# Performance work log

Measured on AMD Instinct MI355X. Metric: run time of the kernel, lower is better.

Reference implementation:

```python
import jax, jax.numpy as jnp
import numpy as np

N_NODES = 100000
N_EDGES = 2000000


def _init_mlp(key, dims, scale=0.05):
    Ws, bs = [], []
    ks = jax.random.split(key, len(dims) - 1)
    for k, di, do in zip(ks, dims[:-1], dims[1:]):
        Ws.append(jax.random.normal(k, (di, do), dtype=jnp.float32) * scale)
        bs.append(jnp.zeros((do,), dtype=jnp.float32))
    return Ws, bs


def setup_inputs() -> dict:
    key = jax.random.key(0)
    ks = jax.random.split(key, 7)
    d = {
        "t": jax.random.uniform(ks[0], (1,), dtype=jnp.float32),
        "x": jax.random.normal(ks[1], (N_NODES, 4), dtype=jnp.float32),
        "Ofixed": jax.random.normal(ks[2], (N_NODES, 2), dtype=jnp.float32),
        "src_idx": jax.random.randint(ks[3], (N_EDGES,), 0, N_NODES, dtype=jnp.int32),
        "tgt_idx": jax.random.randint(ks[4], (N_EDGES,), 0, N_NODES, dtype=jnp.int32),
    }
    # fR: (2*d_O+1)=13 -> [150]*4 -> 50 ; fO: 50 -> [100] -> 4
    R_Ws, R_bs = _init_mlp(ks[5], [13, 150, 150, 150, 150, 50])
    O_Ws, O_bs = _init_mlp(ks[6], [50, 100, 4])
    for i, (W, b) in enumerate(zip(R_Ws, R_bs)):
        d[f"fR_W{i}"] = W
        d[f"fR_b{i}"] = b
    for i, (W, b) in enumerate(zip(O_Ws, O_bs)):
        d[f"fO_W{i}"] = W
        d[f"fO_b{i}"] = b
    return d


def _mlp(h, Ws, bs):
    # hidden layers with ReLU, linear output (matches MLP in the torch code)
    for W, b in zip(Ws[:-1], bs[:-1]):
        h = jax.nn.relu(h @ W + b)
    return h @ Ws[-1] + bs[-1]


def reference(t, x, Ofixed, src_idx, tgt_idx,
              fR_W0, fR_b0, fR_W1, fR_b1, fR_W2, fR_b2, fR_W3, fR_b3, fR_W4, fR_b4,
              fO_W0, fO_b0, fO_W1, fO_b1):
    O = jnp.concatenate([x, Ofixed], axis=1)            # [N, d_O]
    # Msrc.T @ O and Mtgt.T @ O with 0/1 incidence matrices == gathers
    Rsrc = O[src_idx]                                   # [M, d_O]
    Rtgt = O[tgt_idx]                                   # [M, d_O]
    tt = jnp.broadcast_to(t.reshape(1, 1).astype(O.dtype), (src_idx.shape[0], 1))
    R_prime = jnp.concatenate([Rsrc, Rtgt, tt], axis=1)  # [M, 2*d_O+1]
    E = _mlp(R_prime, [fR_W0, fR_W1, fR_W2, fR_W3, fR_W4],
             [fR_b0, fR_b1, fR_b2, fR_b3, fR_b4])        # [M, d_E]
    # Mtgt @ E == scatter-add of edge messages onto target nodes
    E_prime = jax.ops.segment_sum(E, tgt_idx, num_segments=x.shape[0])  # [N, d_E]
    P = _mlp(E_prime, [fO_W0, fO_W1], [fO_b0, fO_b1])    # [N, d_P]
    return P
```

## Files before the change

kernel.cpp:

```cpp
#include <hip/hip_runtime.h>
#include <hip/hip_bf16.h>

typedef unsigned short u16;
typedef __attribute__((ext_vector_type(8))) short short8;
typedef __attribute__((ext_vector_type(4))) float f32x4;

constexpr int SA     = 168;
constexpr int BLK_E  = 64;
constexpr int NTHR   = 192;
constexpr int CHUNK  = 512;
constexpr int WSLOT  = 50 * CHUNK;
constexpr size_t WT_BYTES = 5ull * WSLOT * 2;
constexpr size_t WS_HDR   = 262144;

constexpr int Ls (int s) { return s == 0 ? 0 : (s <= 15 ? 1 + (s - 1) / 5 : 4); }
constexpr int Kss(int s) { return s == 0 ? 0 : (s <= 15 ? (s - 1) % 5 : s - 16); }

__device__ __forceinline__ u16 f2bf(float f) {
    union { float f; unsigned u; } c; c.f = f;
    return (u16)((c.u + 0x7fffu + ((c.u >> 16) & 1u)) >> 16);
}
__device__ __forceinline__ unsigned pk_bf16(float a, float b) {
    float2 f; f.x = a; f.y = b;
    __hip_bfloat162 h = __float22bfloat162_rn(f);
    return *(unsigned*)&h;
}

__device__ __forceinline__ int kperm(int kp) {
    if (kp < 64)  return (kp & 3) * 16 + (kp >> 2);
    if (kp < 128) { const int m = kp - 64;  return (4 + (m & 3)) * 16 + (m >> 2); }
    if (kp < 160) { const int m = kp - 128; return (8 + (m & 1)) * 16 + (m >> 1); }
    return 1 << 30;
}

__global__ void prep_all(const float* __restrict__ W0, const float* __restrict__ W1,
                         const float* __restrict__ W2, const float* __restrict__ W3,
                         const float* __restrict__ W4,
                         const float* __restrict__ B0, const float* __restrict__ B1,
                         const float* __restrict__ B2, const float* __restrict__ B3,
                         const float* __restrict__ B4,
                         u16* __restrict__ Wt, float* __restrict__ Bp)
{
    const int l = blockIdx.y;
    if (l == 5) {
        const int idx = blockIdx.x * blockDim.x + threadIdx.x;
        if (idx < 800) {
            const int ll = idx / 160, j = idx - ll * 160;
            const float* B; int DO;
            if      (ll == 0) { B = B0; DO = 150; }
            else if (ll == 1) { B = B1; DO = 150; }
            else if (ll == 2) { B = B2; DO = 150; }
            else if (ll == 3) { B = B3; DO = 150; }
            else              { B = B4; DO = 50;  }
            Bp[idx] = (j < DO) ? B[j] : 0.f;
        }
        return;
    }
    const float* W; int DI, DO; bool perm;
    if      (l == 0) { W = W0; DI = 13;  DO = 150; perm = false; }
    else if (l == 1) { W = W1; DI = 150; DO = 150; perm = true;  }
    else if (l == 2) { W = W2; DI = 150; DO = 150; perm = true;  }
    else if (l == 3) { W = W3; DI = 150; DO = 150; perm = true;  }
    else             { W = W4; DI = 150; DO = 50;  perm = true;  }
    u16* dst = Wt + (size_t)l * WSLOT;
    for (int idx = blockIdx.x * blockDim.x + threadIdx.x; idx < WSLOT;
         idx += gridDim.x * blockDim.x) {
        const int chunk = idx / CHUNK;
        const int within = idx - chunk * CHUNK;
        const int lane = within >> 3, e = within & 7;
        const int ks = chunk / 10, j = chunk - ks * 10;
        const int c = lane & 15, q = lane >> 4;
        const int n = j * 16 + c;
        const int kphys = ks * 32 + q * 8 + e;
        const int klog = perm ? kperm(kphys) : kphys;
        const float v = (n < DO && klog < DI) ? W[klog * DO + n] : 0.f;
        dst[idx] = f2bf(v);
    }
}

__device__ __forceinline__ void loadB(const u16* __restrict__ Wt, int s,
                                      int wv, int lane, short8 (&slot)[4])
{
    const int l = Ls(s), ks = Kss(s);
    const int jb = (l < 4) ? wv * 4 : 0;
    const int nt = (l < 4 && wv == 2) ? 2 : 4;
    const u16* base = Wt + (size_t)l * WSLOT + (size_t)(ks * 10 + jb) * CHUNK + lane * 8;
#pragma unroll
    for (int jj = 0; jj < 4; ++jj)
        if (jj < nt) slot[jj] = *(const short8*)&base[jj * CHUNK];
}

__device__ __forceinline__ void epilogue(u16* act, const float* __restrict__ Bp,
                                         int l, int wv, int col, int quad,
                                         f32x4 (&acc)[4][4])
{
    const int jb = wv * 4;
    float bb[4];
#pragma unroll
    for (int jj = 0; jj < 4; ++jj) bb[jj] = Bp[l * 160 + (jb + jj) * 16 + col];
#pragma unroll
    for (int mt = 0; mt < 4; ++mt)
#pragma unroll
        for (int r = 0; r < 4; ++r) {
            u16* row = &act[(mt * 16 + quad * 4 + r) * SA];
            if (wv < 2) {
                uint2 pk;
                pk.x = pk_bf16(fmaxf(acc[mt][0][r] + bb[0], 0.f),
                               fmaxf(acc[mt][1][r] + bb[1], 0.f));
                pk.y = pk_bf16(fmaxf(acc[mt][2][r] + bb[2], 0.f),
                               fmaxf(acc[mt][3][r] + bb[3], 0.f));
                *(uint2*)&row[wv * 64 + col * 4] = pk;
            } else {
                *(unsigned*)&row[128 + col * 2] =
                    pk_bf16(fmaxf(acc[mt][0][r] + bb[0], 0.f),
                            fmaxf(acc[mt][1][r] + bb[1], 0.f));
            }
        }
}

__global__ __launch_bounds__(NTHR, 3) void edge_kernel(
    const float* __restrict__ t, const float* __restrict__ x, const float* __restrict__ Ofx,
    const int* __restrict__ src, const int* __restrict__ tgt,
    const u16* __restrict__ Wt, const float* __restrict__ Bp,
    float* __restrict__ Ep, int n_edges, int copy_mask, size_t copy_elems)
{
    __shared__ __align__(16) u16 act[BLK_E * SA];
    __shared__ int tgt_s[BLK_E];

    const int tid  = threadIdx.x;
    const int lane = tid & 63;
    const int wv   = tid >> 6;
    const int col  = lane & 15;
    const int quad = lane >> 4;

    const int xcd = (int)(__builtin_amdgcn_s_getreg(6164) & 7u) & copy_mask;
    float* __restrict__ Epc = Ep + (size_t)xcd * copy_elems;

    short8 Bwin[3][4];
    loadB(Wt, 0, wv, lane, Bwin[0]);
    loadB(Wt, 1, wv, lane, Bwin[1]);
    loadB(Wt, 2, wv, lane, Bwin[2]);

    if (tid < BLK_E) {
        const int e = tid;
        const long long ge = (long long)blockIdx.x * BLK_E + e;
        const bool valid = ge < n_edges;
        const int s = valid ? src[ge] : 0;
        const int g = valid ? tgt[ge] : 0;
        const float4 xs = valid ? *(const float4*)&x[(size_t)s * 4] : float4{0, 0, 0, 0};
        const float2 os = valid ? *(const float2*)&Ofx[(size_t)s * 2] : float2{0, 0};
        const float4 xg = valid ? *(const float4*)&x[(size_t)g * 4] : float4{0, 0, 0, 0};
        const float2 og = valid ? *(const float2*)&Ofx[(size_t)g * 2] : float2{0, 0};
        const float tv = valid ? t[0] : 0.f;
        uint4 w0, w1;
        w0.x = pk_bf16(xs.x, xs.y); w0.y = pk_bf16(xs.z, xs.w);
        w0.z = pk_bf16(os.x, os.y); w0.w = pk_bf16(xg.x, xg.y);
        w1.x = pk_bf16(xg.z, xg.w); w1.y = pk_bf16(og.x, og.y);
        w1.z = pk_bf16(tv, 0.f);    w1.w = 0u;
        u16* row = &act[e * SA];
        *(uint4*)&row[0]  = w0;
        *(uint4*)&row[8]  = w1;
        *(uint4*)&row[16] = uint4{0, 0, 0, 0};
        *(uint4*)&row[24] = uint4{0, 0, 0, 0};
        tgt_s[e] = valid ? g : -1;
    }
    __syncthreads();

    const int ntw = (wv == 2) ? 2 : 4;
    f32x4 acc[4][4];
    short8 Af[4];

#pragma unroll
    for (int mt = 0; mt < 4; ++mt)
#pragma unroll
        for (int jj = 0; jj < 4; ++jj) acc[mt][jj] = f32x4{0.f, 0.f, 0.f, 0.f};
#pragma unroll
    for (int mt = 0; mt < 4; ++mt)
        Af[mt] = *(const short8*)&act[(mt * 16 + col) * SA + quad * 8];
#pragma unroll
    for (int jj = 0; jj < 4; ++jj)
        if (jj < ntw)
#pragma unroll
            for (int mt = 0; mt < 4; ++mt)
                acc[mt][jj] = __builtin_amdgcn_mfma_f32_16x16x32_bf16(
                    Af[mt], Bwin[0][jj], acc[mt][jj], 0, 0, 0);
    loadB(Wt, 3, wv, lane, Bwin[0]);
    __syncthreads();
    epilogue(act, Bp, 0, wv, col, quad, acc);
    __syncthreads();

#pragma unroll
    for (int s = 1; s <= 15; ++s) {
        const int l = 1 + (s - 1) / 5;
        const int ks = (s - 1) % 5;
        const int slot = s % 3;
        if (ks == 0) {
#pragma unroll
            for (int mt = 0; mt < 4; ++mt)
#pragma unroll
                for (int jj = 0; jj < 4; ++jj) acc[mt][jj] = f32x4{0.f, 0.f, 0.f, 0.f};
        }
#pragma unroll
        for (int mt = 0; mt < 4; ++mt)
            Af[mt] = *(const short8*)&act[(mt * 16 + col) * SA + ks * 32 + quad * 8];
#pragma unroll
        for (int jj = 0; jj < 4; ++jj)
            if (jj < ntw)
#pragma unroll
                for (int mt = 0; mt < 4; ++mt)
                    acc[mt][jj] = __builtin_amdgcn_mfma_f32_16x16x32_bf16(
                        Af[mt], Bwin[slot][jj], acc[mt][jj], 0, 0, 0);
        if (s + 3 <= 20) loadB(Wt, s + 3, wv, lane, Bwin[slot]);
        if (ks == 4) {
            __syncthreads();
            epilogue(act, Bp, l, wv, col, quad, acc);
            __syncthreads();
        }
    }

    const int mb  = (wv == 0) ? 0 : wv + 1;
    const int nmt = (wv == 0) ? 2 : 1;
    f32x4 acc4[2][4];
#pragma unroll
    for (int k = 0; k < 2; ++k)
#pragma unroll
        for (int jj = 0; jj < 4; ++jj) acc4[k][jj] = f32x4{0.f, 0.f, 0.f, 0.f};
#pragma unroll
    for (int s = 16; s <= 20; ++s) {
        const int ks = s - 16;
        const int slot = s % 3;
        short8 A4[2];
#pragma unroll
        for (int k = 0; k < 2; ++k)
            if (k < nmt)
                A4[k] = *(const short8*)&act[((mb + k) * 16 + col) * SA + ks * 32 + quad * 8];
#pragma unroll
        for (int jj = 0; jj < 4; ++jj)
#pragma unroll
            for (int k = 0; k < 2; ++k)
                if (k < nmt)
                    acc4[k][jj] = __builtin_amdgcn_mfma_f32_16x16x32_bf16(
                        A4[k], Bwin[slot][jj], acc4[k][jj], 0, 0, 0);
        if (s + 3 <= 20) loadB(Wt, s + 3, wv, lane, Bwin[slot]);
    }

#pragma unroll
    for (int jj = 0; jj < 4; ++jj) {
        const int n = jj * 16 + col;
        if (n < 50) {
            const float bb = Bp[4 * 160 + n];
#pragma unroll
            for (int k = 0; k < 2; ++k)
                if (k < nmt)
#pragma unroll
                    for (int r = 0; r < 4; ++r) {
                        const int g = tgt_s[(mb + k) * 16 + quad * 4 + r];
                        if (g >= 0) atomicAdd(&Epc[(size_t)g * 50 + n], acc4[k][jj][r] + bb);
                    }
        }
    }
}

template<int DI, int DO, bool RELU>
__device__ __forceinline__ void mlp_layer_t(
    const float* __restrict__ W, const float* __restrict__ B,
    float (*in)[64], float (*out)[64], int tid)
{
    const int et = tid & 15;
    const int jt = tid >> 4;
    constexpr int NG = (DO + 15) / 16;

    float acc0[NG], acc1[NG], acc2[NG], acc3[NG];
#pragma unroll
    for (int g = 0; g < NG; ++g) {
        const int j = jt + 16 * g;
        const float bb = (j < DO) ? B[j] : 0.f;
        acc0[g] = bb; acc1[g] = bb; acc2[g] = bb; acc3[g] = bb;
    }
    for (int k = 0; k < DI; ++k) {
        const float4 a = *(const float4*)&in[k][et * 4];
#pragma unroll
        for (int g = 0; g < NG; ++g) {
            const int j = jt + 16 * g;
            const float wv = (j < DO) ? W[k * DO + j] : 0.f;
            acc0[g] = fmaf(a.x, wv, acc0[g]);
            acc1[g] = fmaf(a.y, wv, acc1[g]);
            acc2[g] = fmaf(a.z, wv, acc2[g]);
            acc3[g] = fmaf(a.w, wv, acc3[g]);
        }
    }
#pragma unroll
    for (int g = 0; g < NG; ++g) {
        const int j = jt + 16 * g;
        if (j < DO) {
            float4 v; v.x = acc0[g]; v.y = acc1[g]; v.z = acc2[g]; v.w = acc3[g];
            if (RELU) {
                v.x = fmaxf(v.x, 0.f); v.y = fmaxf(v.y, 0.f);
                v.z = fmaxf(v.z, 0.f); v.w = fmaxf(v.w, 0.f);
            }
            *(float4*)&out[j][et * 4] = v;
        }
    }
}

__global__ __launch_bounds__(256, 2) void node_kernel(
    const float* __restrict__ Ep, int ncopies, size_t copy_elems,
    const float* __restrict__ W0, const float* __restrict__ B0,
    const float* __restrict__ W1, const float* __restrict__ B1,
    float* __restrict__ P, int n_nodes)
{
    __shared__ float bufA[104][64];
    __shared__ float bufB[104][64];
    const int tid = threadIdx.x;
    const int n0  = blockIdx.x * 64;

    for (int idx = tid; idx < 64 * 50; idx += 256) {
        const int e = idx / 50;
        const int k = idx - e * 50;
        const int n = n0 + e;
        float s = 0.f;
        if (n < n_nodes) {
            const float* p = &Ep[(size_t)n * 50 + k];
            for (int c = 0; c < ncopies; ++c) s += p[(size_t)c * copy_elems];
        }
        bufA[k][e] = s;
    }
    __syncthreads();
    mlp_layer_t<50, 100, true >(W0, B0, bufA, bufB, tid); __syncthreads();
    mlp_layer_t<100, 4, false>(W1, B1, bufB, bufA, tid); __syncthreads();
    for (int idx = tid; idx < 64 * 4; idx += 256) {
        const int e = idx & 63;
        const int j = idx >> 6;
        const int n = n0 + e;
        if (n < n_nodes) P[(size_t)n * 4 + j] = bufA[j][e];
    }
}

extern "C" void kernel_launch(void* const* d_in, const int* in_sizes, int n_in,
                              void* d_out, int out_size, void* d_ws, size_t ws_size,
                              hipStream_t stream)
{
    const float* t   = (const float*)d_in[0];
    const float* x   = (const float*)d_in[1];
    const float* Ofx = (const float*)d_in[2];
    const int*   src = (const int*)d_in[3];
    const int*   tgt = (const int*)d_in[4];
    const float* W0  = (const float*)d_in[5];  const float* B0 = (const float*)d_in[6];
    const float* W1  = (const float*)d_in[7];  const float* B1 = (const float*)d_in[8];
    const float* W2  = (const float*)d_in[9];  const float* B2 = (const float*)d_in[10];
    const float* W3  = (const float*)d_in[11]; const float* B3 = (const float*)d_in[12];
    const float* W4  = (const float*)d_in[13]; const float* B4 = (const float*)d_in[14];
    const float* OW0 = (const float*)d_in[15]; const float* OB0 = (const float*)d_in[16];
    const float* OW1 = (const float*)d_in[17]; const float* OB1 = (const float*)d_in[18];

    const int n_nodes = in_sizes[1] / 4;
    const int n_edges = in_sizes[3];

    u16*   Wt = (u16*)d_ws;
    float* Bp = (float*)((char*)d_ws + WT_BYTES);
    float* Ep = (float*)((char*)d_ws + WS_HDR);

    const size_t copy_elems = (size_t)n_nodes * 50;
    const size_t avail = (ws_size > WS_HDR) ? ws_size - WS_HDR : 0;
    int ncopies = 1;
    while (ncopies * 2 <= 2 &&
           (size_t)(ncopies * 2) * copy_elems * sizeof(float) <= avail)
        ncopies *= 2;
    const int copy_mask = ncopies - 1;

    prep_all<<<dim3(32, 6), 256, 0, stream>>>(W0, W1, W2, W3, W4,
                                              B0, B1, B2, B3, B4, Wt, Bp);
    hipMemsetAsync(Ep, 0, (size_t)ncopies * copy_elems * sizeof(float), stream);

    edge_kernel<<<(n_edges + BLK_E - 1) / BLK_E, NTHR, 0, stream>>>(
        t, x, Ofx, src, tgt, Wt, Bp, Ep, n_edges, copy_mask, copy_elems);

    node_kernel<<<(n_nodes + 63) / 64, 256, 0, stream>>>(
        Ep, ncopies, copy_elems, OW0, OB0, OW1, OB1, (float*)d_out, n_nodes);
}
```

Measured before the change: 968.7 us.

## Repartition edge MLP across four waves as 2x2 M/N tiles

Moves the edge kernel from three waves, each owning all 64 rows and a slice of the output columns, to four waves arranged as a 2x2 grid: each wave handles 32 rows by 5 column tiles. The weight K-permutation and the epilogue writes change to fit the new column layout, and the final layer gives each wave one 16-row M tile. The aim is to balance MFMA work evenly across waves, since the old split left the third wave with half the columns, and to lower per-wave accumulator registers so the launch bound can rise to four blocks per SM. In exchange each wave now loads five B fragments per step instead of four, raising per-wave global weight traffic.

Result: no change. 970.2 us (+0.2%).

```diff
diff --git a/kernel.cpp b/kernel.cpp
--- a/kernel.cpp
+++ b/kernel.cpp
@@ -7,7 +7,7 @@
 
 constexpr int SA     = 168;
 constexpr int BLK_E  = 64;
-constexpr int NTHR   = 192;
+constexpr int NTHR   = 256;
 constexpr int CHUNK  = 512;
 constexpr int WSLOT  = 50 * CHUNK;
 constexpr size_t WT_BYTES = 5ull * WSLOT * 2;
@@ -28,8 +28,9 @@
 
 __device__ __forceinline__ int kperm(int kp) {
     if (kp < 64)  return (kp & 3) * 16 + (kp >> 2);
-    if (kp < 128) { const int m = kp - 64;  return (4 + (m & 3)) * 16 + (m >> 2); }
-    if (kp < 160) { const int m = kp - 128; return (8 + (m & 1)) * 16 + (m >> 1); }
+    if (kp < 128) { const int m = kp - 64; return (5 + (m & 3)) * 16 + (m >> 2); }
+    if (kp < 144) return 4 * 16 + (kp - 128);
+    if (kp < 160) return 9 * 16 + (kp - 144);
     return 1 << 30;
 }
 
@@ -79,46 +80,41 @@
 }
 
 __device__ __forceinline__ void loadB(const u16* __restrict__ Wt, int s,
-                                      int wv, int lane, short8 (&slot)[4])
+                                      int ng, int lane, short8 (&slot)[5])
 {
     const int l = Ls(s), ks = Kss(s);
-    const int jb = (l < 4) ? wv * 4 : 0;
-    const int nt = (l < 4 && wv == 2) ? 2 : 4;
+    const int jb = (l < 4) ? ng * 5 : 0;
+    const int nt = (l < 4) ? 5 : 4;
     const u16* base = Wt + (size_t)l * WSLOT + (size_t)(ks * 10 + jb) * CHUNK + lane * 8;
 #pragma unroll
-    for (int jj = 0; jj < 4; ++jj)
+    for (int jj = 0; jj < 5; ++jj)
         if (jj < nt) slot[jj] = *(const short8*)&base[jj * CHUNK];
 }
 
 __device__ __forceinline__ void epilogue(u16* act, const float* __restrict__ Bp,
-                                         int l, int wv, int col, int quad,
-                                         f32x4 (&acc)[4][4])
-{
-    const int jb = wv * 4;
-    float bb[4];
-#pragma unroll
-    for (int jj = 0; jj < 4; ++jj) bb[jj] = Bp[l * 160 + (jb + jj) * 16 + col];
-#pragma unroll
-    for (int mt = 0; mt < 4; ++mt)
+                                         int l, int mg, int ng, int col, int quad,
+                                         f32x4 (&acc)[2][5])
+{
+    float bb[5];
+#pragma unroll
+    for (int jj = 0; jj < 5; ++jj) bb[jj] = Bp[l * 160 + (ng * 5 + jj) * 16 + col];
+#pragma unroll
+    for (int mtl = 0; mtl < 2; ++mtl)
 #pragma unroll
         for (int r = 0; r < 4; ++r) {
-            u16* row = &act[(mt * 16 + quad * 4 + r) * SA];
-            if (wv < 2) {
-                uint2 pk;
-                pk.x = pk_bf16(fmaxf(acc[mt][0][r] + bb[0], 0.f),
-                               fmaxf(acc[mt][1][r] + bb[1], 0.f));
-                pk.y = pk_bf16(fmaxf(acc[mt][2][r] + bb[2], 0.f),
-                               fmaxf(acc[mt][3][r] + bb[3], 0.f));
-                *(uint2*)&row[wv * 64 + col * 4] = pk;
-            } else {
-                *(unsigned*)&row[128 + col * 2] =
-                    pk_bf16(fmaxf(acc[mt][0][r] + bb[0], 0.f),
-                            fmaxf(acc[mt][1][r] + bb[1], 0.f));
-            }
-        }
-}
-
-__global__ __launch_bounds__(NTHR, 3) void edge_kernel(
+            u16* row = &act[((mg * 2 + mtl) * 16 + quad * 4 + r) * SA];
+            uint2 pk;
+            pk.x = pk_bf16(fmaxf(acc[mtl][0][r] + bb[0], 0.f),
+                           fmaxf(acc[mtl][1][r] + bb[1], 0.f));
+            pk.y = pk_bf16(fmaxf(acc[mtl][2][r] + bb[2], 0.f),
+                           fmaxf(acc[mtl][3][r] + bb[3], 0.f));
+            *(uint2*)&row[ng * 64 + col * 4] = pk;
+            row[128 + ng * 16 + col] =
+                (u16)pk_bf16(fmaxf(acc[mtl][4][r] + bb[4], 0.f), 0.f);
+        }
+}
+
+__global__ __launch_bounds__(NTHR, 4) void edge_kernel(
     const float* __restrict__ t, const float* __restrict__ x, const float* __restrict__ Ofx,
     const int* __restrict__ src, const int* __restrict__ tgt,
     const u16* __restrict__ Wt, const float* __restrict__ Bp,
@@ -130,16 +126,18 @@
     const int tid  = threadIdx.x;
     const int lane = tid & 63;
     const int wv   = tid >> 6;
+    const int mg   = wv >> 1;
+    const int ng   = wv & 1;
     const int col  = lane & 15;
     const int quad = lane >> 4;
 
     const int xcd = (int)(__builtin_amdgcn_s_getreg(6164) & 7u) & copy_mask;
     float* __restrict__ Epc = Ep + (size_t)xcd * copy_elems;
 
-    short8 Bwin[3][4];
-    loadB(Wt, 0, wv, lane, Bwin[0]);
-    loadB(Wt, 1, wv, lane, Bwin[1]);
-    loadB(Wt, 2, wv, lane, Bwin[2]);
+    short8 Bwin[3][5];
+    loadB(Wt, 0, ng, lane, Bwin[0]);
+    loadB(Wt, 1, ng, lane, Bwin[1]);
+    loadB(Wt, 2, ng, lane, Bwin[2]);
 
     if (tid < BLK_E) {
         const int e = tid;
@@ -166,27 +164,25 @@
     }
     __syncthreads();
 
-    const int ntw = (wv == 2) ? 2 : 4;
-    f32x4 acc[4][4];
-    short8 Af[4];
-
-#pragma unroll
-    for (int mt = 0; mt < 4; ++mt)
-#pragma unroll
-        for (int jj = 0; jj < 4; ++jj) acc[mt][jj] = f32x4{0.f, 0.f, 0.f, 0.f};
-#pragma unroll
-    for (int mt = 0; mt < 4; ++mt)
-        Af[mt] = *(const short8*)&act[(mt * 16 + col) * SA + quad * 8];
-#pragma unroll
-    for (int jj = 0; jj < 4; ++jj)
-        if (jj < ntw)
-#pragma unroll
-            for (int mt = 0; mt < 4; ++mt)
-                acc[mt][jj] = __builtin_amdgcn_mfma_f32_16x16x32_bf16(
-                    Af[mt], Bwin[0][jj], acc[mt][jj], 0, 0, 0);
-    loadB(Wt, 3, wv, lane, Bwin[0]);
+    f32x4 acc[2][5];
+    short8 Af[2];
+
+#pragma unroll
+    for (int mtl = 0; mtl < 2; ++mtl)
+#pragma unroll
+        for (int jj = 0; jj < 5; ++jj) acc[mtl][jj] = f32x4{0.f, 0.f, 0.f, 0.f};
+#pragma unroll
+    for (int mtl = 0; mtl < 2; ++mtl)
+        Af[mtl] = *(const short8*)&act[((mg * 2 + mtl) * 16 + col) * SA + quad * 8];
+#pragma unroll
+    for (int jj = 0; jj < 5; ++jj)
+#pragma unroll
+        for (int mtl = 0; mtl < 2; ++mtl)
+            acc[mtl][jj] = __builtin_amdgcn_mfma_f32_16x16x32_bf16(
+                Af[mtl], Bwin[0][jj], acc[mtl][jj], 0, 0, 0);
+    loadB(Wt, 3, ng, lane, Bwin[0]);
     __syncthreads();
-    epilogue(act, Bp, 0, wv, col, quad, acc);
+    epilogue(act, Bp, 0, mg, ng, col, quad, acc);
     __syncthreads();
 
 #pragma unroll
@@ -196,52 +192,43 @@
         const int slot = s % 3;
         if (ks == 0) {
 #pragma unroll
-            for (int mt = 0; mt < 4; ++mt)
-#pragma unroll
-                for (int jj = 0; jj < 4; ++jj) acc[mt][jj] = f32x4{0.f, 0.f, 0.f, 0.f};
-        }
-#pragma unroll
-        for (int mt = 0; mt < 4; ++mt)
-            Af[mt] = *(const short8*)&act[(mt * 16 + col) * SA + ks * 32 + quad * 8];
-#pragma unroll
-        for (int jj = 0; jj < 4; ++jj)
-            if (jj < ntw)
-#pragma unroll
-                for (int mt = 0; mt < 4; ++mt)
-                    acc[mt][jj] = __builtin_amdgcn_mfma_f32_16x16x32_bf16(
-                        Af[mt], Bwin[slot][jj], acc[mt][jj], 0, 0, 0);
-        if (s + 3 <= 20) loadB(Wt, s + 3, wv, lane, Bwin[slot]);
+            for (int mtl = 0; mtl < 2; ++mtl)
+#pragma unroll
+                for (int jj = 0; jj < 5; ++jj) acc[mtl][jj] = f32x4{0.f, 0.f, 0.f, 0.f};
+        }
+#pragma unroll
+        for (int mtl = 0; mtl < 2; ++mtl)
+            Af[mtl] = *(const short8*)&act[((mg * 2 + mtl) * 16 + col) * SA
+                                           + ks * 32 + quad * 8];
+#pragma unroll
+        for (int jj = 0; jj < 5; ++jj)
+#pragma unroll
+            for (int mtl = 0; mtl < 2; ++mtl)
+                acc[mtl][jj] = __builtin_amdgcn_mfma_f32_16x16x32_bf16(
+                    Af[mtl], Bwin[slot][jj], acc[mtl][jj], 0, 0, 0);
+        if (s + 3 <= 20) loadB(Wt, s + 3, ng, lane, Bwin[slot]);
         if (ks == 4) {
             __syncthreads();
-            epilogue(act, Bp, l, wv, col, quad, acc);
+            epilogue(act, Bp, l, mg, ng, col, quad, acc);
             __syncthreads();
         }
     }
 
-    const int mb  = (wv == 0) ? 0 : wv + 1;
-    const int nmt = (wv == 0) ? 2 : 1;
-    f32x4 acc4[2][4];
-#pragma unroll
-    for (int k = 0; k < 2; ++k)
-#pragma unroll
-        for (int jj = 0; jj < 4; ++jj) acc4[k][jj] = f32x4{0.f, 0.f, 0.f, 0.f};
+    const int mt4 = mg * 2 + ng;
+    f32x4 acc4[4];
+#pragma unroll
+    for (int jj = 0; jj < 4; ++jj) acc4[jj] = f32x4{0.f, 0.f, 0.f, 0.f};
 #pragma unroll
     for (int s = 16; s <= 20; ++s) {
         const int ks = s - 16;
         const int slot = s % 3;
-        short8 A4[2];
-#pragma unroll
-        for (int k = 0; k < 2; ++k)
-            if (k < nmt)
-                A4[k] = *(const short8*)&act[((mb + k) * 16 + col) * SA + ks * 32 + quad * 8];
+        const short8 A4 = *(const short8*)&act[(mt4 * 16 + col) * SA
+                                               + ks * 32 + quad * 8];
 #pragma unroll
         for (int jj = 0; jj < 4; ++jj)
-#pragma unroll
-            for (int k = 0; k < 2; ++k)
-                if (k < nmt)
-                    acc4[k][jj] = __builtin_amdgcn_mfma_f32_16x16x32_bf16(
-                        A4[k], Bwin[slot][jj], acc4[k][jj], 0, 0, 0);
-        if (s + 3 <= 20) loadB(Wt, s + 3, wv, lane, Bwin[slot]);
+            acc4[jj] = __builtin_amdgcn_mfma_f32_16x16x32_bf16(
+                A4, Bwin[slot][jj], acc4[jj], 0, 0, 0);
+        if (s + 3 <= 20) loadB(Wt, s + 3, ng, lane, Bwin[slot]);
     }
 
 #pragma unroll
@@ -250,13 +237,10 @@
         if (n < 50) {
             const float bb = Bp[4 * 160 + n];
 #pragma unroll
-            for (int k = 0; k < 2; ++k)
-                if (k < nmt)
-#pragma unroll
-                    for (int r = 0; r < 4; ++r) {
-                        const int g = tgt_s[(mb + k) * 16 + quad * 4 + r];
-                        if (g >= 0) atomicAdd(&Epc[(size_t)g * 50 + n], acc4[k][jj][r] + bb);
-                    }
+            for (int r = 0; r < 4; ++r) {
+                const int g = tgt_s[mt4 * 16 + quad * 4 + r];
+                if (g >= 0) atomicAdd(&Epc[(size_t)g * 50 + n], acc4[jj][r] + bb);
+            }
         }
     }
 }
```
